# Kernel optimization log

Hardware: AMD Instinct MI355X
Metric: run time of the kernel (lower is better)

## Reference

```python
import jax, jax.numpy as jnp
import numpy as np

M1, M2, M3 = 12, 12, 8
WIDTH = 32


def _spectral_conv(v, wr, wi):
    # v: [B, C, X, Y, T]; wr/wi: [4, Ci, Co, M1, M2, M3]
    B, C, X, Y, T = v.shape
    vft = jnp.fft.rfftn(v, axes=(-3, -2, -1))  # [B,C,X,Y,T//2+1] complex
    w = wr.astype(jnp.complex64) + 1j * wi.astype(jnp.complex64)
    mul = lambda blk, ww: jnp.einsum('bixyz,ioxyz->boxyz', blk, ww)
    out = jnp.zeros((B, wr.shape[2], X, Y, T // 2 + 1), dtype=vft.dtype)
    out = out.at[:, :, :M1, :M2, :M3].set(mul(vft[:, :, :M1, :M2, :M3], w[0]))
    out = out.at[:, :, -M1:, :M2, :M3].set(mul(vft[:, :, -M1:, :M2, :M3], w[1]))
    out = out.at[:, :, :M1, -M2:, :M3].set(mul(vft[:, :, :M1, -M2:, :M3], w[2]))
    out = out.at[:, :, -M1:, -M2:, :M3].set(mul(vft[:, :, -M1:, -M2:, :M3], w[3]))
    return jnp.fft.irfftn(out, s=(X, Y, T), axes=(-3, -2, -1))


def _conv1x1(v, w, b):
    # v: [B,C,X,Y,T]; w: [Co,Ci]; b: [Co]
    return jnp.einsum('bixyz,oi->boxyz', v, w) + b[None, :, None, None, None]


def setup_inputs() -> dict:
    key = jax.random.key(0)
    ks = jax.random.split(key, 24)
    B, X, Y, T = 8, 64, 64, 40
    W = WIDTH
    scale = 1.0 / (W * W)
    d = {}
    d['h'] = jax.random.normal(ks[0], (B, X, Y, T, 2), dtype=jnp.float32)
    d['x'] = jax.random.normal(ks[1], (B, X, Y, T, 3), dtype=jnp.float32)
    d['fc0_w'] = jax.random.normal(ks[2], (5, W), dtype=jnp.float32) * 0.3
    d['fc0_b'] = jnp.zeros((W,), dtype=jnp.float32)
    for i, name in enumerate(['sc0', 'sc1', 'sc3']):
        d[name + '_wr'] = scale * jax.random.uniform(ks[3 + 2 * i], (4, W, W, M1, M2, M3), dtype=jnp.float32)
        d[name + '_wi'] = scale * jax.random.uniform(ks[4 + 2 * i], (4, W, W, M1, M2, M3), dtype=jnp.float32)
    for i, name in enumerate(['w0', 'w1', 'w3']):
        d[name + '_w'] = jax.random.normal(ks[9 + 2 * i], (W, W), dtype=jnp.float32) * (1.0 / np.sqrt(W))
        d[name + '_b'] = jnp.zeros((W,), dtype=jnp.float32)
    d['fc1_w'] = jax.random.normal(ks[15], (W, 64), dtype=jnp.float32) * (1.0 / np.sqrt(W))
    d['fc1_b'] = jnp.zeros((64,), dtype=jnp.float32)
    d['fc2_w'] = jax.random.normal(ks[16], (64, 2), dtype=jnp.float32) * 0.125
    d['fc2_b'] = jnp.zeros((2,), dtype=jnp.float32)
    return d


def reference(h, x, fc0_w, fc0_b, sc0_wr, sc0_wi, sc1_wr, sc1_wi, sc3_wr, sc3_wi,
              w0_w, w0_b, w1_w, w1_b, w3_w, w3_b, fc1_w, fc1_b, fc2_w, fc2_b):
    v = jnp.concatenate((h, x), axis=-1)                 # [B,X,Y,T,5]
    v = v @ fc0_w + fc0_b                                # lift to width
    v = jnp.transpose(v, (0, 4, 1, 2, 3))                # [B,W,X,Y,T]
    v = jax.nn.gelu(_spectral_conv(v, sc0_wr, sc0_wi) + _conv1x1(v, w0_w, w0_b), approximate=False)
    v = jax.nn.gelu(_spectral_conv(v, sc1_wr, sc1_wi) + _conv1x1(v, w1_w, w1_b), approximate=False)
    v = _spectral_conv(v, sc3_wr, sc3_wi) + _conv1x1(v, w3_w, w3_b)
    v = jnp.transpose(v, (0, 2, 3, 4, 1))                # [B,X,Y,T,W]
    v = jax.nn.gelu(v @ fc1_w + fc1_b, approximate=False)
    return v @ fc2_w + fc2_b                             # [B,X,Y,T,2]
```

## Files before the change

kernel.cpp:

```cpp
#include <hip/hip_runtime.h>
#include <math.h>

#define BATCH 8
#define WID   32
#define NX    64
#define NY    64
#define NT    40
#define M1C   12
#define KT    8
#define KXC   24
#define KYC   24
#define NXY   (NX*NY)
#define NXYT  (NXY*NT)
#define NP    (BATCH*NXYT)

#define TWO_PI 6.283185307179586f

static __device__ __forceinline__ float gelu_f(float v){
  return 0.5f*v*(1.0f + erff(v*0.7071067811865476f));
}

static __device__ __forceinline__ void barrier_lds(){
  asm volatile("s_waitcnt lgkmcnt(0)\n\ts_barrier" ::: "memory");
}


__global__ __launch_bounds__(256) void k_fc0(const float* __restrict__ h, const float* __restrict__ x,
                                             const float* __restrict__ w, const float* __restrict__ b,
                                             float* __restrict__ V){
  __shared__ float sw[160], sb[32];
  int tid=threadIdx.x;
  if(tid<160) sw[tid]=w[tid];
  if(tid<32)  sb[tid]=b[tid];
  __syncthreads();
  int pl = tid>>3, q = tid&7;
  int p = blockIdx.x*32 + pl;
  float i0=h[(size_t)p*2], i1=h[(size_t)p*2+1];
  float i2=x[(size_t)p*3], i3=x[(size_t)p*3+1], i4=x[(size_t)p*3+2];
  int c0=q*4;
  float4 o;
  float* po=(float*)&o;
  #pragma unroll
  for(int u=0;u<4;u++){
    int c=c0+u;
    po[u] = sb[c] + i0*sw[c] + i1*sw[32+c] + i2*sw[64+c] + i3*sw[96+c] + i4*sw[128+c];
  }
  ((float4*)V)[(size_t)p*8 + q] = o;
}

__global__ __launch_bounds__(256) void k_fwd_ty(const float* __restrict__ V, float2* __restrict__ F2){
  __shared__ __align__(16) unsigned char smem[61696];
  float*  vt    = (float*)smem;
  float2* f2out = (float2*)smem;
  float2* twy   = (float2*)(smem + 49408);
  int tid = threadIdx.x;
  int b = blockIdx.x >> 6, x = blockIdx.x & 63;
  int c = tid & 31, k = tid >> 5;
  for(int i=tid;i<KYC*NY;i+=256){
    int ky=i/NY, y=i-ky*NY;
    int f = ky<M1C ? ky : ky+40;
    float ang = -TWO_PI*(float)((f*y)%NY)/(float)NY;
    twy[ky*NY+y] = make_float2(cosf(ang), sinf(ang));
  }
  float2 twr[NT];
  #pragma unroll
  for(int t=0;t<NT;t++){
    float ang = -TWO_PI*(float)((k*t)%NT)/(float)NT;
    twr[t] = make_float2(cosf(ang), sinf(ang));
  }
  float2 acc[KYC];
  #pragma unroll
  for(int ky=0;ky<KYC;ky++) acc[ky]=make_float2(0.f,0.f);
  const float4* src = (const float4*)(V + (size_t)(b*NX+x)*(NY*NT*WID));
  for(int g=0; g<8; g++){
    __syncthreads();
    #pragma unroll
    for(int r=0;r<10;r++) ((float4*)vt)[r*256+tid] = src[g*2560 + r*256 + tid];
    __syncthreads();
    for(int yl=0; yl<8; yl+=2){
      float sr0=0.f, si0=0.f, sr1=0.f, si1=0.f;
      const float* vp0 = vt + yl*1280 + c;
      const float* vp1 = vp0 + 1280;
      #pragma unroll
      for(int t=0;t<NT;t++){
        float2 w = twr[t];
        float v0 = vp0[t*32];
        float v1 = vp1[t*32];
        sr0 += v0*w.x; si0 += v0*w.y;
        sr1 += v1*w.x; si1 += v1*w.y;
      }
      int y = g*8 + yl;
      #pragma unroll
      for(int ky=0;ky<KYC;ky++){
        float4 wy = *(const float4*)&twy[ky*NY + y];
        acc[ky].x += sr0*wy.x - si0*wy.y + sr1*wy.z - si1*wy.w;
        acc[ky].y += sr0*wy.y + si0*wy.x + sr1*wy.w + si1*wy.z;
      }
    }
  }
  __syncthreads();
  #pragma unroll
  for(int ky=0;ky<KYC;ky++) f2out[c*193 + ky*KT + k] = acc[ky];
  __syncthreads();
  for(int i=tid;i<WID*KYC*KT;i+=256){
    int cc=i/192, e=i-cc*192;
    F2[((size_t)(b*WID+cc)*NX + x)*(KYC*KT) + e] = f2out[cc*193 + e];
  }
}

__global__ __launch_bounds__(256) void k_fwd_x(const float2* __restrict__ F2, float2* __restrict__ F3){
  __shared__ float2 tile[NX*KT];
  __shared__ float2 twi[KXC*65];
  int tid=threadIdx.x;
  int bc = blockIdx.x / KYC;
  int ky = blockIdx.x - bc*KYC;
  for(int i=tid;i<NX*KT;i+=256){
    int xx=i/KT, kt=i-xx*KT;
    tile[i] = F2[((size_t)bc*NX + xx)*(KYC*KT) + ky*KT + kt];
  }
  for(int i=tid;i<KXC*NX;i+=256){
    int kx=i/NX, xx=i-kx*NX;
    int f = kx<M1C ? kx : kx+40;
    float ang = -TWO_PI*(float)((f*xx)%NX)/(float)NX;
    twi[kx*65+xx] = make_float2(cosf(ang), sinf(ang));
  }
  __syncthreads();
  for(int item=tid; item<KXC*KT; item+=256){
    int kx=item/KT, kt=item-kx*KT;
    float sr=0.f, si=0.f;
    #pragma unroll 8
    for(int xx=0;xx<NX;xx++){
      float2 a = tile[xx*KT+kt];
      float2 w = twi[kx*65+xx];
      sr += a.x*w.x - a.y*w.y;
      si += a.x*w.y + a.y*w.x;
    }
    F3[(size_t)bc*(KXC*KYC*KT) + kx*(KYC*KT) + ky*KT + kt] = make_float2(sr,si);
  }
}

__global__ __launch_bounds__(256) void k_mix(const float2* __restrict__ F3, const float* __restrict__ wr,
                                             const float* __restrict__ wi, float2* __restrict__ F4){
  __shared__ float2 f3s[BATCH*WID*KT];
  int tid = threadIdx.x;
  int kx = blockIdx.x / KYC, ky = blockIdx.x - kx*KYC;
  int mode0 = blockIdx.x * KT;
  int xp = (kx>=M1C), yp = (ky>=M1C);
  int m1 = kx - M1C*xp, m2 = ky - M1C*yp;
  int blk = xp + 2*yp;
  for(int i=tid;i<1024;i+=256){
    int row=i>>2, q=i&3;
    ((float4*)f3s)[row*4+q] = ((const float4*)(F3 + (size_t)row*4608 + mode0))[q];
  }
  int o = tid>>3, kt = tid&7;
  size_t wbase = (size_t)blk*1179648 + (size_t)o*1152 + m1*96 + m2*8 + kt;
  float wre[WID], wim[WID];
  #pragma unroll
  for(int i=0;i<WID;i++){
    wre[i] = wr[wbase + (size_t)i*36864];
    wim[i] = wi[wbase + (size_t)i*36864];
  }
  __syncthreads();
  #pragma unroll
  for(int b=0;b<BATCH;b++){
    float ar=0.f, ai=0.f;
    #pragma unroll
    for(int i=0;i<WID;i++){
      float2 a = f3s[(b*WID+i)*KT + kt];
      ar += a.x*wre[i] - a.y*wim[i];
      ai += a.x*wim[i] + a.y*wre[i];
    }
    F4[(size_t)(b*WID+o)*4608 + mode0 + kt] = make_float2(ar,ai);
  }
}

__global__ __launch_bounds__(256) void k_inv_x(const float2* __restrict__ F4, float2* __restrict__ F2){
  __shared__ float2 tile[KXC*KT];
  __shared__ float2 twi[NX*25];
  int tid=threadIdx.x;
  int bc = blockIdx.x / KYC, ky = blockIdx.x - (blockIdx.x/KYC)*KYC;
  for(int i=tid;i<KXC*KT;i+=256){
    int kx=i/KT, kt=i-kx*KT;
    tile[i] = F4[(size_t)bc*4608 + kx*(KYC*KT) + ky*KT + kt];
  }
  for(int i=tid;i<NX*KXC;i+=256){
    int xx=i/KXC, kx=i-xx*KXC;
    int f = kx<M1C ? kx : kx+40;
    float ang = TWO_PI*(float)((f*xx)%NX)/(float)NX;
    twi[xx*25+kx] = make_float2(cosf(ang)*(1.0f/64.0f), sinf(ang)*(1.0f/64.0f));
  }
  __syncthreads();
  for(int item=tid; item<NX*KT; item+=256){
    int xx=item/KT, kt=item-xx*KT;
    float sr=0.f, si=0.f;
    #pragma unroll 8
    for(int kx=0;kx<KXC;kx++){
      float2 a = tile[kx*KT+kt];
      float2 w = twi[xx*25+kx];
      sr += a.x*w.x - a.y*w.y;
      si += a.x*w.y + a.y*w.x;
    }
    F2[((size_t)bc*NX + xx)*(KYC*KT) + ky*KT + kt] = make_float2(sr,si);
  }
}

template<bool GELU>
__global__ __launch_bounds__(256) void k_conv(const float2* __restrict__ F2, const float* __restrict__ wcv,
                                              const float* __restrict__ bcv, float* __restrict__ V){
  __shared__ __align__(16) unsigned char smem[24576];
  float*  vt0  = (float*)smem;
  float*  vt1  = (float*)(smem+5120);
  float2* ftc  = (float2*)(smem+10240);
  float2* tcts = (float2*)(smem+12288);
  float2* twy  = (float2*)(smem+14848);
  float2* f2h  = (float2*)smem;

  int tid=threadIdx.x;
  int b  = blockIdx.x >> 7;
  int x  = (blockIdx.x >> 1) & 63;
  int y0 = (blockIdx.x & 1) * 32;
  int cid = tid & 31, ktid = tid >> 5;
  int oid = tid & 31, tg  = tid >> 5;

  float2 fr[KYC];
  #pragma unroll
  for(int half=0; half<2; half++){
    for(int i=tid;i<1536;i+=256){
      int cc=i/96, q=i-cc*96;
      ((float4*)f2h)[i] = *((const float4*)(F2 + ((size_t)(b*WID + half*16 + cc)*NX + x)*(KYC*KT)) + q);
    }
    __syncthreads();
    if((cid>>4) == half){
      const float2* fp = f2h + (cid&15)*192 + ktid;
      #pragma unroll
      for(int ky=0;ky<KYC;ky++) fr[ky] = fp[ky*8];
    }
    __syncthreads();
  }
  float wreg[WID];
  #pragma unroll
  for(int cc=0;cc<WID;cc++) wreg[cc] = wcv[oid*WID + cc];
  float breg = bcv[oid];
  for(int i=tid;i<KT*NT;i+=256){
    int k=i/NT, t=i-k*NT;
    float ang = TWO_PI*(float)((k*t)%NT)/(float)NT;
    float sc = (k==0 ? 1.0f : 2.0f)*(1.0f/(float)NT);
    tcts[i] = make_float2(cosf(ang)*sc, sinf(ang)*sc);
  }
  for(int i=tid;i<32*KYC;i+=256){
    int yy=i/KYC, ky=i-yy*KYC;
    int f = ky<M1C ? ky : ky+40;
    float ang = TWO_PI*(float)((f*(y0+yy))%NY)/(float)NY;
    twy[i] = make_float2(cosf(ang)*(1.0f/64.0f), sinf(ang)*(1.0f/64.0f));
  }
  float* plane = V + (size_t)((b*NX+x)*NY + y0)*(NT*WID);
  const float4* gp = (const float4*)plane;
  bool has2 = tid < 64;
  float4 g0 = gp[tid];
  float4 g1 = has2 ? gp[256+tid] : make_float4(0,0,0,0);
  ((float4*)vt0)[tid] = g0;
  if(has2) ((float4*)vt0)[256+tid] = g1;
  __syncthreads();

  for(int y=0;y<32;y++){
    if(y+1 < 32){
      g0 = gp[(size_t)(y+1)*320 + tid];
      if(has2) g1 = gp[(size_t)(y+1)*320 + 256 + tid];
    }
    {
      const float2* tw = twy + y*KYC;
      float sr=0.f, si=0.f;
      #pragma unroll
      for(int ky=0;ky<KYC;ky++){
        float2 w = tw[ky];
        float2 a = fr[ky];
        sr += a.x*w.x - a.y*w.y;
        si += a.x*w.y + a.y*w.x;
      }
      ftc[ktid*32 + cid] = make_float2(sr,si);
    }
    barrier_lds();
    {
      float2 fR[KT];
      #pragma unroll
      for(int k=0;k<KT;k++) fR[k] = ftc[k*32 + oid];
      const float* vb = (y&1) ? vt1 : vt0;
      float* outp = plane + (size_t)y*(NT*WID);
      #pragma unroll
      for(int j=0;j<5;j++){
        int t = tg*5 + j;
        float a = breg;
        const float* vrow = vb + t*32;
        #pragma unroll
        for(int c4=0;c4<WID;c4+=4){
          float4 vv = *(const float4*)(vrow + c4);
          a += vv.x*wreg[c4] + vv.y*wreg[c4+1] + vv.z*wreg[c4+2] + vv.w*wreg[c4+3];
        }
        #pragma unroll
        for(int k=0;k<KT;k++){
          float2 w = tcts[k*NT + t];
          a += fR[k].x*w.x - fR[k].y*w.y;
        }
        outp[t*32 + oid] = GELU ? gelu_f(a) : a;
      }
    }
    if(y+1 < 32){
      float* d = (y&1) ? vt0 : vt1;
      ((float4*)d)[tid] = g0;
      if(has2) ((float4*)d)[256+tid] = g1;
    }
    barrier_lds();
  }
}

__global__ __launch_bounds__(256) void k_mlp(const float* __restrict__ V, const float* __restrict__ w1,
                                             const float* __restrict__ b1, const float* __restrict__ w2,
                                             const float* __restrict__ b2, float* __restrict__ out){
  __shared__ float sw1t[64*WID];
  __shared__ float sb1[64], sw2[128], sb2[2];
  int tid=threadIdx.x;
  for(int i=tid;i<64*WID;i+=256){ int j=i>>5, c=i&31; sw1t[i]=w1[c*64+j]; }
  if(tid<64) sb1[tid]=b1[tid];
  if(tid<128) sw2[tid]=w2[tid];
  if(tid<2) sb2[tid]=b2[tid];
  __syncthreads();
  size_t p0 = (size_t)blockIdx.x*1024 + (size_t)tid*4;
  float vv[128];
  const float4* vp = (const float4*)(V + p0*WID);
  #pragma unroll
  for(int q=0;q<32;q++) *((float4*)(vv+4*q)) = vp[q];
  float oa[8];
  #pragma unroll
  for(int pt=0;pt<4;pt++){ oa[2*pt]=sb2[0]; oa[2*pt+1]=sb2[1]; }
  #pragma unroll 4
  for(int j=0;j<64;j++){
    float a0=sb1[j], a1=a0, a2=a0, a3=a0;
    const float* wrow = sw1t + j*WID;
    #pragma unroll
    for(int c4=0;c4<WID;c4+=4){
      float4 w = *(const float4*)(wrow + c4);
      a0 += vv[     c4]*w.x + vv[     c4+1]*w.y + vv[     c4+2]*w.z + vv[     c4+3]*w.w;
      a1 += vv[32 + c4]*w.x + vv[32 + c4+1]*w.y + vv[32 + c4+2]*w.z + vv[32 + c4+3]*w.w;
      a2 += vv[64 + c4]*w.x + vv[64 + c4+1]*w.y + vv[64 + c4+2]*w.z + vv[64 + c4+3]*w.w;
      a3 += vv[96 + c4]*w.x + vv[96 + c4+1]*w.y + vv[96 + c4+2]*w.z + vv[96 + c4+3]*w.w;
    }
    a0=gelu_f(a0); a1=gelu_f(a1); a2=gelu_f(a2); a3=gelu_f(a3);
    float u0=sw2[2*j], u1=sw2[2*j+1];
    oa[0]+=a0*u0; oa[1]+=a0*u1; oa[2]+=a1*u0; oa[3]+=a1*u1;
    oa[4]+=a2*u0; oa[5]+=a2*u1; oa[6]+=a3*u0; oa[7]+=a3*u1;
  }
  float4* op = (float4*)(out + p0*2);
  op[0]=make_float4(oa[0],oa[1],oa[2],oa[3]);
  op[1]=make_float4(oa[4],oa[5],oa[6],oa[7]);
}

extern "C" void kernel_launch(void* const* d_in, const int* in_sizes, int n_in,
                              void* d_out, int out_size, void* d_ws, size_t ws_size,
                              hipStream_t stream){
  const float* h     = (const float*)d_in[0];
  const float* x     = (const float*)d_in[1];
  const float* fc0_w = (const float*)d_in[2];
  const float* fc0_b = (const float*)d_in[3];
  const float* scwr[3] = {(const float*)d_in[4], (const float*)d_in[6], (const float*)d_in[8]};
  const float* scwi[3] = {(const float*)d_in[5], (const float*)d_in[7], (const float*)d_in[9]};
  const float* cw[3]   = {(const float*)d_in[10], (const float*)d_in[12], (const float*)d_in[14]};
  const float* cb[3]   = {(const float*)d_in[11], (const float*)d_in[13], (const float*)d_in[15]};
  const float* fc1_w = (const float*)d_in[16];
  const float* fc1_b = (const float*)d_in[17];
  const float* fc2_w = (const float*)d_in[18];
  const float* fc2_b = (const float*)d_in[19];

  const size_t VSZ = (size_t)BATCH*WID*NXYT;
  float*  V  = (float*)d_ws;
  float2* F2 = (float2*)(V + VSZ);
  float2* F4 = F2 + (size_t)BATCH*WID*NX*KYC*KT;
  float2* F3 = (float2*)d_out;

  k_fc0<<<NP/32, 256, 0, stream>>>(h, x, fc0_w, fc0_b, V);
  for(int L=0; L<3; L++){
    k_fwd_ty<<<BATCH*NX, 256, 0, stream>>>(V, F2);
    k_fwd_x<<<(BATCH*WID)*KYC, 256, 0, stream>>>(F2, F3);
    k_mix<<<KXC*KYC, 256, 0, stream>>>(F3, scwr[L], scwi[L], F4);
    k_inv_x<<<(BATCH*WID)*KYC, 256, 0, stream>>>(F4, F2);
    if(L<2) k_conv<true ><<<BATCH*NX*2, 256, 0, stream>>>(F2, cw[L], cb[L], V);
    else    k_conv<false><<<BATCH*NX*2, 256, 0, stream>>>(F2, cw[L], cb[L], V);
  }
  k_mlp<<<NP/1024, 256, 0, stream>>>(V, fc1_w, fc1_b, fc2_w, fc2_b, (float*)d_out);
}
```

Before: 1.587 ms.

## Register-tile k_conv output as 5x4 blocks and process four y rows per barrier

Restructures the final stage of k_conv so each thread computes a 5-time by 4-channel output tile, reading the 1x1 weights and the T-axis inverse-DFT twiddles from shared memory as float4 instead of keeping a 32-float weight row in registers. It also processes four y rows per iteration, one per wavefront, with a register-staged prefetch of the next four rows, which cuts barriers from 64 to 16 per block. Output stores become float4-wide. The cost is more shared memory traffic for weights and a larger register footprint from acc[5][4] and vreg[5], which may lower occupancy.

```diff
diff --git a/kernel.cpp b/kernel.cpp
--- a/kernel.cpp
+++ b/kernel.cpp
@@ -204,23 +204,27 @@
   }
 }
 
+#define VT_OFF 0
+#define WT_OFF 5760
+#define TX_OFF 6784
+#define SX_OFF 7584
+#define TW_OFF 9632
+#define BB_OFF 11168
 template<bool GELU>
 __global__ __launch_bounds__(256) void k_conv(const float2* __restrict__ F2, const float* __restrict__ wcv,
                                               const float* __restrict__ bcv, float* __restrict__ V){
-  __shared__ __align__(16) unsigned char smem[24576];
-  float*  vt0  = (float*)smem;
-  float*  vt1  = (float*)(smem+5120);
-  float2* ftc  = (float2*)(smem+10240);
-  float2* tcts = (float2*)(smem+12288);
-  float2* twy  = (float2*)(smem+14848);
-  float2* f2h  = (float2*)smem;
+  __shared__ __align__(16) float smem[11200];
+  float2* f2h = (float2*)smem;
+  float2* twy = (float2*)(smem + TW_OFF);
 
   int tid=threadIdx.x;
   int b  = blockIdx.x >> 7;
   int x  = (blockIdx.x >> 1) & 63;
   int y0 = (blockIdx.x & 1) * 32;
   int cid = tid & 31, ktid = tid >> 5;
-  int oid = tid & 31, tg  = tid >> 5;
+  int w   = tid >> 6;
+  int lane = tid & 63;
+  int tq = lane >> 3, og = lane & 7;
 
   float2 fr[KYC];
   #pragma unroll
@@ -237,15 +241,16 @@
     }
     __syncthreads();
   }
-  float wreg[WID];
-  #pragma unroll
-  for(int cc=0;cc<WID;cc++) wreg[cc] = wcv[oid*WID + cc];
-  float breg = bcv[oid];
-  for(int i=tid;i<KT*NT;i+=256){
-    int k=i/NT, t=i-k*NT;
-    float ang = TWO_PI*(float)((k*t)%NT)/(float)NT;
-    float sc = (k==0 ? 1.0f : 2.0f)*(1.0f/(float)NT);
-    tcts[i] = make_float2(cosf(ang)*sc, sinf(ang)*sc);
+  for(int i=tid;i<1024;i+=256){
+    int cc=i>>5, oo=i&31;
+    smem[WT_OFF + cc*32 + oo] = wcv[oo*32 + cc];
+  }
+  for(int i=tid;i<640;i+=256){
+    int t=i>>4, kk=i&15;
+    int kt = kk&7;
+    float sc = (kt==0 ? 1.0f : 2.0f)*(1.0f/(float)NT);
+    float ang = TWO_PI*(float)((kt*t)%NT)/(float)NT;
+    smem[TX_OFF + t*20 + kk] = (kk<8) ? cosf(ang)*sc : -sinf(ang)*sc;
   }
   for(int i=tid;i<32*KYC;i+=256){
     int yy=i/KYC, ky=i-yy*KYC;
@@ -253,61 +258,94 @@
     float ang = TWO_PI*(float)((f*(y0+yy))%NY)/(float)NY;
     twy[i] = make_float2(cosf(ang)*(1.0f/64.0f), sinf(ang)*(1.0f/64.0f));
   }
+  if(tid<32) smem[BB_OFF+tid] = bcv[tid];
+
   float* plane = V + (size_t)((b*NX+x)*NY + y0)*(NT*WID);
-  const float4* gp = (const float4*)plane;
-  bool has2 = tid < 64;
-  float4 g0 = gp[tid];
-  float4 g1 = has2 ? gp[256+tid] : make_float4(0,0,0,0);
-  ((float4*)vt0)[tid] = g0;
-  if(has2) ((float4*)vt0)[256+tid] = g1;
-  __syncthreads();
-
-  for(int y=0;y<32;y++){
-    if(y+1 < 32){
-      g0 = gp[(size_t)(y+1)*320 + tid];
-      if(has2) g1 = gp[(size_t)(y+1)*320 + 256 + tid];
+  const float4* plane4 = (const float4*)plane;
+  float4 vreg[5];
+  #pragma unroll
+  for(int k=0;k<5;k++) vreg[k] = plane4[tid + k*256];
+  __syncthreads();
+
+  for(int q=0;q<8;q++){
+    #pragma unroll
+    for(int k=0;k<5;k++){
+      int f4 = tid + k*256;
+      int dy = f4/320; int r4 = f4 - dy*320;
+      int t = r4>>3, c4 = r4&7;
+      *(float4*)&smem[VT_OFF + dy*1440 + t*36 + c4*4] = vreg[k];
+    }
+    #pragma unroll
+    for(int dy=0;dy<4;dy++){
+      const float2* twp = twy + (q*4+dy)*KYC;
+      float sr=0.f, si=0.f;
+      #pragma unroll
+      for(int ky=0;ky<KYC;ky++){
+        float2 wv = twp[ky];
+        float2 a = fr[ky];
+        sr += a.x*wv.x - a.y*wv.y;
+        si += a.x*wv.y + a.y*wv.x;
+      }
+      smem[SX_OFF + dy*512 + ktid*32 + cid]       = sr;
+      smem[SX_OFF + dy*512 + 256 + ktid*32 + cid] = si;
+    }
+    barrier_lds();
+    if(q<7){
+      #pragma unroll
+      for(int k=0;k<5;k++) vreg[k] = plane4[(q+1)*1280 + tid + k*256];
     }
     {
-      const float2* tw = twy + y*KYC;
-      float sr=0.f, si=0.f;
-      #pragma unroll
-      for(int ky=0;ky<KYC;ky++){
-        float2 w = tw[ky];
-        float2 a = fr[ky];
-        sr += a.x*w.x - a.y*w.y;
-        si += a.x*w.y + a.y*w.x;
-      }
-      ftc[ktid*32 + cid] = make_float2(sr,si);
-    }
-    barrier_lds();
-    {
-      float2 fR[KT];
-      #pragma unroll
-      for(int k=0;k<KT;k++) fR[k] = ftc[k*32 + oid];
-      const float* vb = (y&1) ? vt1 : vt0;
-      float* outp = plane + (size_t)y*(NT*WID);
+      int yy = q*4 + w;
+      const float* vtp = &smem[VT_OFF + w*1440];
+      const float* sxp = &smem[SX_OFF + w*512];
+      float4 bb4 = *(const float4*)&smem[BB_OFF + og*4];
+      float acc[5][4];
       #pragma unroll
       for(int j=0;j<5;j++){
-        int t = tg*5 + j;
-        float a = breg;
-        const float* vrow = vb + t*32;
+        acc[j][0]=bb4.x; acc[j][1]=bb4.y; acc[j][2]=bb4.z; acc[j][3]=bb4.w;
+      }
+      #pragma unroll
+      for(int c4=0;c4<8;c4++){
+        float4 w0 = *(const float4*)&smem[WT_OFF + (c4*4+0)*32 + og*4];
+        float4 w1 = *(const float4*)&smem[WT_OFF + (c4*4+1)*32 + og*4];
+        float4 w2 = *(const float4*)&smem[WT_OFF + (c4*4+2)*32 + og*4];
+        float4 w3 = *(const float4*)&smem[WT_OFF + (c4*4+3)*32 + og*4];
         #pragma unroll
-        for(int c4=0;c4<WID;c4+=4){
-          float4 vv = *(const float4*)(vrow + c4);
-          a += vv.x*wreg[c4] + vv.y*wreg[c4+1] + vv.z*wreg[c4+2] + vv.w*wreg[c4+3];
+        for(int j=0;j<5;j++){
+          float4 v4 = *(const float4*)&vtp[(tq*5+j)*36 + c4*4];
+          acc[j][0] += v4.x*w0.x + v4.y*w1.x + v4.z*w2.x + v4.w*w3.x;
+          acc[j][1] += v4.x*w0.y + v4.y*w1.y + v4.z*w2.y + v4.w*w3.y;
+          acc[j][2] += v4.x*w0.z + v4.y*w1.z + v4.z*w2.z + v4.w*w3.z;
+          acc[j][3] += v4.x*w0.w + v4.y*w1.w + v4.z*w2.w + v4.w*w3.w;
         }
+      }
+      #pragma unroll
+      for(int k4=0;k4<4;k4++){
+        float4 s0 = *(const float4*)&sxp[(k4*4+0)*32 + og*4];
+        float4 s1 = *(const float4*)&sxp[(k4*4+1)*32 + og*4];
+        float4 s2 = *(const float4*)&sxp[(k4*4+2)*32 + og*4];
+        float4 s3 = *(const float4*)&sxp[(k4*4+3)*32 + og*4];
         #pragma unroll
-        for(int k=0;k<KT;k++){
-          float2 w = tcts[k*NT + t];
-          a += fR[k].x*w.x - fR[k].y*w.y;
+        for(int j=0;j<5;j++){
+          float4 t4 = *(const float4*)&smem[TX_OFF + (tq*5+j)*20 + k4*4];
+          acc[j][0] += t4.x*s0.x + t4.y*s1.x + t4.z*s2.x + t4.w*s3.x;
+          acc[j][1] += t4.x*s0.y + t4.y*s1.y + t4.z*s2.y + t4.w*s3.y;
+          acc[j][2] += t4.x*s0.z + t4.y*s1.z + t4.z*s2.z + t4.w*s3.z;
+          acc[j][3] += t4.x*s0.w + t4.y*s1.w + t4.z*s2.w + t4.w*s3.w;
         }
-        outp[t*32 + oid] = GELU ? gelu_f(a) : a;
-      }
-    }
-    if(y+1 < 32){
-      float* d = (y&1) ? vt0 : vt1;
-      ((float4*)d)[tid] = g0;
-      if(has2) ((float4*)d)[256+tid] = g1;
+      }
+      #pragma unroll
+      for(int j=0;j<5;j++){
+        int t = tq*5+j;
+        float4 o4;
+        if(GELU){
+          o4.x=gelu_f(acc[j][0]); o4.y=gelu_f(acc[j][1]);
+          o4.z=gelu_f(acc[j][2]); o4.w=gelu_f(acc[j][3]);
+        }else{
+          o4.x=acc[j][0]; o4.y=acc[j][1]; o4.z=acc[j][2]; o4.w=acc[j][3];
+        }
+        *(float4*)(plane + (size_t)yy*1280 + t*32 + og*4) = o4;
+      }
     }
     barrier_lds();
   }
```

Measured after the change: 1.989 ms. 1.25x slower.
